# Optimization experiments

Hardware: AMD Instinct MI355X
Metric: run time of the kernel (lower is better)

Reference implementation:

```python
import jax, jax.numpy as jnp
import numpy as np

VOCAB = 1000
H = 500  # embedding_size == hidden_size
NEG_SLOPE = 0.01  # nn.LeakyReLU default


def lstm_last_hidden(tokens, emb, Wih, Whh, bih, bhh):
    # tokens: [N, L] int; returns final hidden state [N, H] (batch_first LSTM, h_T)
    x = emb[tokens]  # [N, L, H]
    N = x.shape[0]
    h0 = jnp.zeros((N, H), x.dtype)

    def step(carry, xt):
        h, c = carry
        gates = xt @ Wih.T + h @ Whh.T + bih + bhh  # [N, 4H], torch gate order i,f,g,o
        i, f, g, o = jnp.split(gates, 4, axis=-1)
        c = jax.nn.sigmoid(f) * c + jax.nn.sigmoid(i) * jnp.tanh(g)
        h = jax.nn.sigmoid(o) * jnp.tanh(c)
        return (h, c), None

    (h, _), _ = jax.lax.scan(step, (h0, h0), jnp.swapaxes(x, 0, 1))
    return h


def setup_inputs() -> dict:
    key = jax.random.key(0)
    ks = jax.random.split(key, 16)
    B, L, NH = 256, 128, 2048
    goals = jax.random.randint(ks[0], (B, L), 0, VOCAB, dtype=jnp.int32)
    hyps = jax.random.randint(ks[1], (NH, L), 0, VOCAB, dtype=jnp.int32)
    segment_ids = jnp.sort(jax.random.randint(ks[2], (NH,), 0, B, dtype=jnp.int32))
    s = 1.0 / np.sqrt(H)
    emb = jax.random.normal(ks[3], (VOCAB, H), jnp.float32)
    Wih = jax.random.uniform(ks[4], (4 * H, H), jnp.float32, -s, s)
    Whh = jax.random.uniform(ks[5], (4 * H, H), jnp.float32, -s, s)
    bih = jax.random.uniform(ks[6], (4 * H,), jnp.float32, -s, s)
    bhh = jax.random.uniform(ks[7], (4 * H,), jnp.float32, -s, s)
    s1 = 1.0 / np.sqrt(2 * H)
    W1 = jax.random.uniform(ks[8], (H, 2 * H), jnp.float32, -s1, s1)
    b1 = jax.random.uniform(ks[9], (H,), jnp.float32, -s1, s1)
    W2 = jax.random.uniform(ks[10], (H, H), jnp.float32, -s, s)
    b2 = jax.random.uniform(ks[11], (H,), jnp.float32, -s, s)
    Wf = jax.random.uniform(ks[12], (H, H), jnp.float32, -s, s)
    bf = jax.random.uniform(ks[13], (H,), jnp.float32, -s, s)
    return {"goals": goals, "hyps": hyps, "segment_ids": segment_ids,
            "emb": emb, "Wih": Wih, "Whh": Whh, "bih": bih, "bhh": bhh,
            "W1": W1, "b1": b1, "W2": W2, "b2": b2, "Wf": Wf, "bf": bf}


def reference(goals, hyps, segment_ids, emb, Wih, Whh, bih, bhh, W1, b1, W2, b2, Wf, bf):
    B = goals.shape[0]
    g = lstm_last_hidden(goals, emb, Wih, Whh, bih, bhh)      # [B, H]
    h = lstm_last_hidden(hyps, emb, Wih, Whh, bih, bhh)       # [NH, H]
    hyp_sum = jax.ops.segment_sum(h, segment_ids, num_segments=B)  # [B, H]
    x = jnp.concatenate([g, hyp_sum], axis=1)                  # [B, 2H]
    lrelu = lambda z: jnp.where(z >= 0, z, NEG_SLOPE * z)
    x = lrelu(x @ W1.T + b1)
    x = lrelu(x @ W2.T + b2)
    x = x @ Wf.T + bf
    norm = jnp.maximum(jnp.linalg.norm(x, axis=1, keepdims=True), 1e-12)
    return x / norm
```

## Files before the change

kernel.cpp:

```cpp
#include <hip/hip_runtime.h>
#include <hip/hip_bf16.h>

#define HH 500
#define G4 2000
#define NSEQ 2304
#define NGOALS 256
#define NHYPS 2048
#define LSEQ 128
#define NVOCAB 1000
#define NEG_SLOPE 0.01f

typedef __attribute__((ext_vector_type(4))) float f32x4;
typedef __attribute__((ext_vector_type(8))) short short8;

__device__ __forceinline__ float sigm(float x) { return 1.0f / (1.0f + expf(-x)); }

__device__ __forceinline__ void gload_lds16(const void* g, void* l) {
    __builtin_amdgcn_global_load_lds(
        (const __attribute__((address_space(1))) unsigned int*)g,
        (__attribute__((address_space(3))) unsigned int*)l, 16, 0, 0);
}

__global__ void gemm_at_bt(const float* __restrict__ A, const float* __restrict__ B,
                           const float* __restrict__ bias, const float* __restrict__ bias2,
                           float* __restrict__ C, int M, int N, int K, int act)
{
    __shared__ float as[32][17];
    __shared__ float bs[32][17];
    int tid = threadIdx.x;
    int tx = tid & 15, ty = tid >> 4;
    int m0 = blockIdx.y * 32, n0 = blockIdx.x * 32;
    float acc[2][2] = {};
    for (int k0 = 0; k0 < K; k0 += 16) {
        #pragma unroll
        for (int i = 0; i < 2; ++i) {
            int idx = i * 256 + tid;
            int r = idx >> 4, k = idx & 15;
            int gm = m0 + r, gk = k0 + k;
            as[r][k] = (gm < M && gk < K) ? A[gm * K + gk] : 0.0f;
            int gn = n0 + r;
            bs[r][k] = (gn < N && gk < K) ? B[gn * K + gk] : 0.0f;
        }
        __syncthreads();
        #pragma unroll
        for (int kk = 0; kk < 16; ++kk) {
            float a0 = as[ty][kk], a1 = as[ty + 16][kk];
            float b0 = bs[tx][kk], b1 = bs[tx + 16][kk];
            acc[0][0] += a0 * b0; acc[0][1] += a0 * b1;
            acc[1][0] += a1 * b0; acc[1][1] += a1 * b1;
        }
        __syncthreads();
    }
    #pragma unroll
    for (int i = 0; i < 2; ++i) {
        int m = m0 + ty + i * 16;
        if (m >= M) continue;
        #pragma unroll
        for (int j = 0; j < 2; ++j) {
            int n = n0 + tx + j * 16;
            if (n >= N) continue;
            float v = acc[i][j];
            if (bias)  v += bias[n];
            if (bias2) v += bias2[n];
            if (act == 1) v = (v >= 0.0f) ? v : NEG_SLOPE * v;
            C[m * N + n] = v;
        }
    }
}

__global__ void conv_whh(const float* __restrict__ Whh, __hip_bfloat16* __restrict__ Wb)
{
    int idx = blockIdx.x * 256 + threadIdx.x;
    if (idx >= 4 * 512 * 512) return;
    int k = idx & 511, u = (idx >> 9) & 511, g = idx >> 18;
    float v = (u < HH && k < HH) ? Whh[(g * HH + u) * HH + k] : 0.0f;
    Wb[idx] = __float2bfloat16(v);
}

__global__ __launch_bounds__(256) void lstm_step_mfma(
    const float* __restrict__ T,
    const int* __restrict__ goals, const int* __restrict__ hyps,
    const __hip_bfloat16* __restrict__ Wb,
    const __hip_bfloat16* __restrict__ hin,
    __hip_bfloat16* __restrict__ hout,
    float* __restrict__ c, int t)
{
    __shared__ char lds[20480];
    char* As = lds;
    char* Bs = lds + 4096;
    int tid = threadIdx.x, w = tid >> 6, lane = tid & 63;
    int n0 = blockIdx.y * 32, u0 = blockIdx.x * 32;
    f32x4 acc[4] = {};

    int lrow = lane >> 3;
    int cblk = (lane & 7) ^ lrow;
    const short* hin_s = (const short*)hin;
    const short* wb_s  = (const short*)Wb;

    int nsub = (w >> 1) * 16, usub = (w & 1) * 16;
    int arow = nsub + (lane & 15);
    int r7 = lane & 7;

    for (int k0 = 0; k0 < 512; k0 += 64) {
        gload_lds16(hin_s + (size_t)(n0 + w * 8 + lrow) * 512 + k0 + cblk * 8,
                    As + w * 1024);
        #pragma unroll
        for (int i = 0; i < 4; ++i) {
            int r = (i * 4 + w) * 8 + lrow;
            int g = r >> 5, u = u0 + (r & 31);
            gload_lds16(wb_s + (size_t)(g * 512 + u) * 512 + k0 + cblk * 8,
                        Bs + (i * 4 + w) * 1024);
        }
        __syncthreads();
        #pragma unroll
        for (int ks = 0; ks < 2; ++ks) {
            int blk = (ks * 4 + (lane >> 4)) ^ r7;
            short8 a = *(const short8*)(As + arow * 128 + blk * 16);
            #pragma unroll
            for (int g = 0; g < 4; ++g) {
                int br = g * 32 + usub + (lane & 15);
                short8 b = *(const short8*)(Bs + br * 128 + blk * 16);
                acc[g] = __builtin_amdgcn_mfma_f32_16x16x32_bf16(a, b, acc[g], 0, 0, 0);
            }
        }
        __syncthreads();
    }

    int u = u0 + usub + (lane & 15);
    if (u < HH) {
        #pragma unroll
        for (int r = 0; r < 4; ++r) {
            int n = n0 + nsub + (lane >> 4) * 4 + r;
            int tok = (n < NGOALS) ? goals[n * LSEQ + t] : hyps[(n - NGOALS) * LSEQ + t];
            const float* Trow = T + (size_t)tok * G4;
            float gi = acc[0][r] + Trow[u];
            float gf = acc[1][r] + Trow[HH + u];
            float gg = acc[2][r] + Trow[2 * HH + u];
            float go = acc[3][r] + Trow[3 * HH + u];
            float si = sigm(gi), sf = sigm(gf), so = sigm(go);
            float cv = c[(size_t)n * 512 + u];
            cv = sf * cv + si * tanhf(gg);
            c[(size_t)n * 512 + u] = cv;
            hout[(size_t)n * 512 + u] = __float2bfloat16(so * tanhf(cv));
        }
    }
}

__global__ void segsum_bf(const __hip_bfloat16* __restrict__ hfin,
                          const int* __restrict__ segid, float* __restrict__ hyp_sum)
{
    int row = blockIdx.y;
    int u = blockIdx.x * 256 + threadIdx.x;
    if (u >= HH) return;
    int b = segid[row];
    atomicAdd(&hyp_sum[b * HH + u],
              __bfloat162float(hfin[(size_t)(NGOALS + row) * 512 + u]));
}

__global__ void concat_bf(const __hip_bfloat16* __restrict__ hfin,
                          const float* __restrict__ hyp_sum, float* __restrict__ xcat)
{
    int r = blockIdx.y;
    int k = blockIdx.x * 256 + threadIdx.x;
    if (k >= 2 * HH) return;
    xcat[r * 2 * HH + k] = (k < HH) ? __bfloat162float(hfin[(size_t)r * 512 + k])
                                    : hyp_sum[r * HH + (k - HH)];
}

__global__ void rownorm(const float* __restrict__ X, float* __restrict__ out)
{
    __shared__ float red[256];
    int r = blockIdx.x;
    int tid = threadIdx.x;
    float v0 = (tid < HH) ? X[r * HH + tid] : 0.0f;
    float v1 = (tid + 256 < HH) ? X[r * HH + tid + 256] : 0.0f;
    red[tid] = v0 * v0 + v1 * v1;
    __syncthreads();
    for (int st = 128; st > 0; st >>= 1) {
        if (tid < st) red[tid] += red[tid + st];
        __syncthreads();
    }
    float nrm = fmaxf(sqrtf(red[0]), 1e-12f);
    if (tid < HH) out[r * HH + tid] = v0 / nrm;
    if (tid + 256 < HH) out[r * HH + tid + 256] = v1 / nrm;
}

extern "C" void kernel_launch(void* const* d_in, const int* in_sizes, int n_in,
                              void* d_out, int out_size, void* d_ws, size_t ws_size,
                              hipStream_t stream)
{
    const int*   goals = (const int*)d_in[0];
    const int*   hyps  = (const int*)d_in[1];
    const int*   segid = (const int*)d_in[2];
    const float* emb   = (const float*)d_in[3];
    const float* Wih   = (const float*)d_in[4];
    const float* Whh   = (const float*)d_in[5];
    const float* bih   = (const float*)d_in[6];
    const float* bhh   = (const float*)d_in[7];
    const float* W1    = (const float*)d_in[8];
    const float* b1    = (const float*)d_in[9];
    const float* W2    = (const float*)d_in[10];
    const float* b2    = (const float*)d_in[11];
    const float* Wf    = (const float*)d_in[12];
    const float* bf    = (const float*)d_in[13];
    float* out = (float*)d_out;

    char* base = (char*)d_ws;
    float*          T    = (float*)(base + 0);
    __hip_bfloat16* Wb   = (__hip_bfloat16*)(base + 8000000);
    __hip_bfloat16* hb0  = (__hip_bfloat16*)(base + 10097152);
    __hip_bfloat16* hb1  = (__hip_bfloat16*)(base + 12456448);
    float*          c    = (float*)(base + 14815744);
    float*          hsum = (float*)(base + 19534336);
    float*          xcat = (float*)(base + 20046336);
    float*          x1   = (float*)(base + 21070336);
    float*          x2   = (float*)(base + 21582336);

    gemm_at_bt<<<dim3((G4 + 31) / 32, (NVOCAB + 31) / 32), 256, 0, stream>>>(
        emb, Wih, bih, bhh, T, NVOCAB, G4, HH, 0);
    conv_whh<<<4096, 256, 0, stream>>>(Whh, Wb);

    hipMemsetAsync(hb0,  0, 2359296, stream);
    hipMemsetAsync(hb1,  0, 2359296, stream);
    hipMemsetAsync(c,    0, 4718592, stream);
    hipMemsetAsync(hsum, 0,  512000, stream);

    __hip_bfloat16* hb[2] = { hb0, hb1 };
    for (int t = 0; t < LSEQ; ++t) {
        lstm_step_mfma<<<dim3(16, NSEQ / 32), 256, 0, stream>>>(
            T, goals, hyps, Wb, hb[t & 1], hb[(t + 1) & 1], c, t);
    }
    __hip_bfloat16* hfin = hb0;

    segsum_bf<<<dim3(2, NHYPS), 256, 0, stream>>>(hfin, segid, hsum);
    concat_bf<<<dim3(4, NGOALS), 256, 0, stream>>>(hfin, hsum, xcat);

    gemm_at_bt<<<dim3(16, 8), 256, 0, stream>>>(xcat, W1, b1, nullptr, x1, NGOALS, HH, 2 * HH, 1);
    gemm_at_bt<<<dim3(16, 8), 256, 0, stream>>>(x1,   W2, b2, nullptr, x2, NGOALS, HH, HH, 1);
    gemm_at_bt<<<dim3(16, 8), 256, 0, stream>>>(x2,   Wf, bf, nullptr, xcat, NGOALS, HH, HH, 0);
    rownorm<<<NGOALS, 256, 0, stream>>>(xcat, out);
}
```

Baseline: 2.333 ms.

## Retile LSTM step with 32x32 MFMA double-buffered single-wave blocks and split-bf16 table GEMM

Replaces the per-step recurrent kernel with a single-wavefront block that computes a 64x(4x32) tile using 32x32x16 bf16 MFMAs. Global-to-LDS loads are double-buffered so the next K chunk loads while the current one is computed. The input-projection table is now built with a bf16 hi/lo split MFMA GEMM instead of the scalar fp32 GEMM, and its rows are padded to 512 columns per gate. The step kernel now launches 576 single-wave blocks each step, which lowers occupancy per CU and raises register pressure from the larger accumulators.

```diff
diff --git a/kernel.cpp b/kernel.cpp
--- a/kernel.cpp
+++ b/kernel.cpp
@@ -10,8 +10,9 @@
 #define NVOCAB 1000
 #define NEG_SLOPE 0.01f
 
-typedef __attribute__((ext_vector_type(4))) float f32x4;
-typedef __attribute__((ext_vector_type(8))) short short8;
+typedef __attribute__((ext_vector_type(4)))  float f32x4;
+typedef __attribute__((ext_vector_type(16))) float f32x16;
+typedef __attribute__((ext_vector_type(8)))  short short8;
 
 __device__ __forceinline__ float sigm(float x) { return 1.0f / (1.0f + expf(-x)); }
 
@@ -19,6 +20,182 @@
     __builtin_amdgcn_global_load_lds(
         (const __attribute__((address_space(1))) unsigned int*)g,
         (__attribute__((address_space(3))) unsigned int*)l, 16, 0, 0);
+}
+
+__global__ void split_emb(const float* __restrict__ emb,
+                          __hip_bfloat16* __restrict__ Eh, __hip_bfloat16* __restrict__ El)
+{
+    int idx = blockIdx.x * 256 + threadIdx.x;
+    if (idx >= 1024 * 512) return;
+    int k = idx & 511, r = idx >> 9;
+    float v = (r < NVOCAB && k < HH) ? emb[r * HH + k] : 0.0f;
+    __hip_bfloat16 h = __float2bfloat16(v);
+    Eh[idx] = h;
+    El[idx] = __float2bfloat16(v - __bfloat162float(h));
+}
+
+__global__ void split_wih(const float* __restrict__ Wih,
+                          __hip_bfloat16* __restrict__ Wh, __hip_bfloat16* __restrict__ Wl)
+{
+    int idx = blockIdx.x * 256 + threadIdx.x;
+    if (idx >= 2000 * 512) return;
+    int k = idx & 511, r = idx >> 9;
+    float v = (k < HH) ? Wih[r * HH + k] : 0.0f;
+    __hip_bfloat16 h = __float2bfloat16(v);
+    Wh[idx] = h;
+    Wl[idx] = __float2bfloat16(v - __bfloat162float(h));
+}
+
+__global__ void conv_whh(const float* __restrict__ Whh, __hip_bfloat16* __restrict__ Wb)
+{
+    int idx = blockIdx.x * 256 + threadIdx.x;
+    if (idx >= 4 * 512 * 512) return;
+    int k = idx & 511, u = (idx >> 9) & 511, g = idx >> 18;
+    float v = (u < HH && k < HH) ? Whh[(g * HH + u) * HH + k] : 0.0f;
+    Wb[idx] = __float2bfloat16(v);
+}
+
+__global__ __launch_bounds__(256) void tgemm_split(
+    const __hip_bfloat16* __restrict__ Eh, const __hip_bfloat16* __restrict__ El,
+    const __hip_bfloat16* __restrict__ Wh, const __hip_bfloat16* __restrict__ Wl,
+    const float* __restrict__ bih, const float* __restrict__ bhh,
+    float* __restrict__ T4)
+{
+    __shared__ char lds[40960];
+    int tid = threadIdx.x, w = tid >> 6, lane = tid & 63;
+    int j0 = blockIdx.x * 16;
+    int m0 = blockIdx.y * 64;
+    int lrow = lane >> 3, cblk = (lane & 7) ^ lrow, r7 = lane & 7;
+    const short* eh = (const short*)Eh; const short* el = (const short*)El;
+    const short* wh = (const short*)Wh; const short* wl = (const short*)Wl;
+    f32x4 acc = {};
+    int arow = w * 16 + (lane & 15);
+
+    auto STAGE = [&](int buf, int k0) {
+        char* base = lds + buf * 20480;
+        #pragma unroll
+        for (int i = 0; i < 2; ++i) {
+            int r = (w * 2 + i) * 8 + lrow;
+            gload_lds16(eh + (size_t)(m0 + r) * 512 + k0 + cblk * 8, base + (w * 2 + i) * 1024);
+            gload_lds16(el + (size_t)(m0 + r) * 512 + k0 + cblk * 8, base + 8192 + (w * 2 + i) * 1024);
+        }
+        {
+            int half = w & 1;
+            int r = half * 8 + lrow;
+            const short* src = (w < 2) ? wh : wl;
+            int off = (w < 2) ? 16384 : 18432;
+            gload_lds16(src + (size_t)(j0 + r) * 512 + 0 + cblk * 8 + k0, base + off + half * 1024);
+        }
+    };
+
+    STAGE(0, 0);
+    __syncthreads();
+    int cur = 0;
+    for (int ch = 0; ch < 8; ++ch) {
+        if (ch < 7) STAGE(cur ^ 1, (ch + 1) * 64);
+        char* base = lds + cur * 20480;
+        #pragma unroll
+        for (int ks = 0; ks < 2; ++ks) {
+            int blk = (ks * 4 + (lane >> 4)) ^ r7;
+            short8 ah = *(const short8*)(base + arow * 128 + blk * 16);
+            short8 al = *(const short8*)(base + 8192 + arow * 128 + blk * 16);
+            short8 bh = *(const short8*)(base + 16384 + (lane & 15) * 128 + blk * 16);
+            short8 bl = *(const short8*)(base + 18432 + (lane & 15) * 128 + blk * 16);
+            acc = __builtin_amdgcn_mfma_f32_16x16x32_bf16(ah, bh, acc, 0, 0, 0);
+            acc = __builtin_amdgcn_mfma_f32_16x16x32_bf16(ah, bl, acc, 0, 0, 0);
+            acc = __builtin_amdgcn_mfma_f32_16x16x32_bf16(al, bh, acc, 0, 0, 0);
+        }
+        if (ch < 7) { __syncthreads(); cur ^= 1; }
+    }
+    int j = j0 + (lane & 15);
+    int g = (j >= 1500) ? 3 : (j >= 1000) ? 2 : (j >= 500) ? 1 : 0;
+    int u = j - g * 500;
+    float bias = bih[j] + bhh[j];
+    #pragma unroll
+    for (int r = 0; r < 4; ++r) {
+        int m = m0 + w * 16 + (lane >> 4) * 4 + r;
+        if (m < NVOCAB) T4[(size_t)m * 2048 + g * 512 + u] = acc[r] + bias;
+    }
+}
+
+__global__ __launch_bounds__(64) void lstm_step3(
+    const float* __restrict__ T4,
+    const int* __restrict__ goals, const int* __restrict__ hyps,
+    const __hip_bfloat16* __restrict__ Wb,
+    const __hip_bfloat16* __restrict__ hin,
+    __hip_bfloat16* __restrict__ hout,
+    float* __restrict__ c, int tstep)
+{
+    __shared__ char lds[49152];
+    int lane = threadIdx.x;
+    int u0 = blockIdx.x * 32, n0 = blockIdx.y * 64;
+    int lrow = lane >> 3, l7 = lane & 7;
+    const short* hin_s = (const short*)hin;
+    const short* wb_s  = (const short*)Wb;
+    f32x16 acc[2][4] = {};
+
+    auto STAGE = [&](int buf, int k0) {
+        char* As_ = lds + buf * 24576;
+        char* Bs_ = As_ + 8192;
+        #pragma unroll
+        for (int i = 0; i < 8; ++i) {
+            int cb = l7 ^ lrow ^ (i & 3);
+            gload_lds16(hin_s + (size_t)(n0 + i * 8 + lrow) * 512 + k0 + cb * 8, As_ + i * 1024);
+        }
+        #pragma unroll
+        for (int i = 0; i < 16; ++i) {
+            int cb = l7 ^ lrow ^ (i & 3);
+            int r = i * 8 + lrow;
+            int g = r >> 5, uu = r & 31;
+            gload_lds16(wb_s + (size_t)(g * 512 + u0 + uu) * 512 + k0 + cb * 8, Bs_ + i * 1024);
+        }
+    };
+
+    STAGE(0, 0);
+    __syncthreads();
+    int cur = 0;
+    int l31 = lane & 31;
+    int keybase = l7 ^ ((lane >> 3) & 3);
+    for (int ch = 0; ch < 8; ++ch) {
+        if (ch < 7) STAGE(cur ^ 1, (ch + 1) * 64);
+        char* As_ = lds + cur * 24576;
+        char* Bs_ = As_ + 8192;
+        #pragma unroll
+        for (int ks = 0; ks < 4; ++ks) {
+            int blk = (ks * 2 + (lane >> 5)) ^ keybase;
+            short8 a0 = *(const short8*)(As_ + l31 * 128 + blk * 16);
+            short8 a1 = *(const short8*)(As_ + (32 + l31) * 128 + blk * 16);
+            #pragma unroll
+            for (int g = 0; g < 4; ++g) {
+                short8 b = *(const short8*)(Bs_ + (g * 32 + l31) * 128 + blk * 16);
+                acc[0][g] = __builtin_amdgcn_mfma_f32_32x32x16_bf16(a0, b, acc[0][g], 0, 0, 0);
+                acc[1][g] = __builtin_amdgcn_mfma_f32_32x32x16_bf16(a1, b, acc[1][g], 0, 0, 0);
+            }
+        }
+        if (ch < 7) { __syncthreads(); cur ^= 1; }
+    }
+
+    int u = u0 + l31;
+    if (u < HH) {
+        #pragma unroll
+        for (int r = 0; r < 2; ++r) {
+            #pragma unroll
+            for (int reg = 0; reg < 16; ++reg) {
+                int n = n0 + r * 32 + (reg & 3) + 8 * (reg >> 2) + 4 * (lane >> 5);
+                int tok = (n < NGOALS) ? goals[n * LSEQ + tstep] : hyps[(n - NGOALS) * LSEQ + tstep];
+                const float* Tg = T4 + (size_t)tok * 2048;
+                float gi = acc[r][0][reg] + Tg[u];
+                float gf = acc[r][1][reg] + Tg[512 + u];
+                float gg = acc[r][2][reg] + Tg[1024 + u];
+                float go = acc[r][3][reg] + Tg[1536 + u];
+                float si = sigm(gi), sf = sigm(gf), so = sigm(go);
+                float cv = c[(size_t)n * 512 + u];
+                cv = sf * cv + si * tanhf(gg);
+                c[(size_t)n * 512 + u] = cv;
+                hout[(size_t)n * 512 + u] = __float2bfloat16(so * tanhf(cv));
+            }
+        }
+    }
 }
 
 __global__ void gemm_at_bt(const float* __restrict__ A, const float* __restrict__ B,
@@ -64,84 +241,6 @@
             if (bias2) v += bias2[n];
             if (act == 1) v = (v >= 0.0f) ? v : NEG_SLOPE * v;
             C[m * N + n] = v;
-        }
-    }
-}
-
-__global__ void conv_whh(const float* __restrict__ Whh, __hip_bfloat16* __restrict__ Wb)
-{
-    int idx = blockIdx.x * 256 + threadIdx.x;
-    if (idx >= 4 * 512 * 512) return;
-    int k = idx & 511, u = (idx >> 9) & 511, g = idx >> 18;
-    float v = (u < HH && k < HH) ? Whh[(g * HH + u) * HH + k] : 0.0f;
-    Wb[idx] = __float2bfloat16(v);
-}
-
-__global__ __launch_bounds__(256) void lstm_step_mfma(
-    const float* __restrict__ T,
-    const int* __restrict__ goals, const int* __restrict__ hyps,
-    const __hip_bfloat16* __restrict__ Wb,
-    const __hip_bfloat16* __restrict__ hin,
-    __hip_bfloat16* __restrict__ hout,
-    float* __restrict__ c, int t)
-{
-    __shared__ char lds[20480];
-    char* As = lds;
-    char* Bs = lds + 4096;
-    int tid = threadIdx.x, w = tid >> 6, lane = tid & 63;
-    int n0 = blockIdx.y * 32, u0 = blockIdx.x * 32;
-    f32x4 acc[4] = {};
-
-    int lrow = lane >> 3;
-    int cblk = (lane & 7) ^ lrow;
-    const short* hin_s = (const short*)hin;
-    const short* wb_s  = (const short*)Wb;
-
-    int nsub = (w >> 1) * 16, usub = (w & 1) * 16;
-    int arow = nsub + (lane & 15);
-    int r7 = lane & 7;
-
-    for (int k0 = 0; k0 < 512; k0 += 64) {
-        gload_lds16(hin_s + (size_t)(n0 + w * 8 + lrow) * 512 + k0 + cblk * 8,
-                    As + w * 1024);
-        #pragma unroll
-        for (int i = 0; i < 4; ++i) {
-            int r = (i * 4 + w) * 8 + lrow;
-            int g = r >> 5, u = u0 + (r & 31);
-            gload_lds16(wb_s + (size_t)(g * 512 + u) * 512 + k0 + cblk * 8,
-                        Bs + (i * 4 + w) * 1024);
-        }
-        __syncthreads();
-        #pragma unroll
-        for (int ks = 0; ks < 2; ++ks) {
-            int blk = (ks * 4 + (lane >> 4)) ^ r7;
-            short8 a = *(const short8*)(As + arow * 128 + blk * 16);
-            #pragma unroll
-            for (int g = 0; g < 4; ++g) {
-                int br = g * 32 + usub + (lane & 15);
-                short8 b = *(const short8*)(Bs + br * 128 + blk * 16);
-                acc[g] = __builtin_amdgcn_mfma_f32_16x16x32_bf16(a, b, acc[g], 0, 0, 0);
-            }
-        }
-        __syncthreads();
-    }
-
-    int u = u0 + usub + (lane & 15);
-    if (u < HH) {
-        #pragma unroll
-        for (int r = 0; r < 4; ++r) {
-            int n = n0 + nsub + (lane >> 4) * 4 + r;
-            int tok = (n < NGOALS) ? goals[n * LSEQ + t] : hyps[(n - NGOALS) * LSEQ + t];
-            const float* Trow = T + (size_t)tok * G4;
-            float gi = acc[0][r] + Trow[u];
-            float gf = acc[1][r] + Trow[HH + u];
-            float gg = acc[2][r] + Trow[2 * HH + u];
-            float go = acc[3][r] + Trow[3 * HH + u];
-            float si = sigm(gi), sf = sigm(gf), so = sigm(go);
-            float cv = c[(size_t)n * 512 + u];
-            cv = sf * cv + si * tanhf(gg);
-            c[(size_t)n * 512 + u] = cv;
-            hout[(size_t)n * 512 + u] = __float2bfloat16(so * tanhf(cv));
         }
     }
 }
@@ -206,19 +305,24 @@
     float* out = (float*)d_out;
 
     char* base = (char*)d_ws;
-    float*          T    = (float*)(base + 0);
-    __hip_bfloat16* Wb   = (__hip_bfloat16*)(base + 8000000);
-    __hip_bfloat16* hb0  = (__hip_bfloat16*)(base + 10097152);
-    __hip_bfloat16* hb1  = (__hip_bfloat16*)(base + 12456448);
-    float*          c    = (float*)(base + 14815744);
-    float*          hsum = (float*)(base + 19534336);
-    float*          xcat = (float*)(base + 20046336);
-    float*          x1   = (float*)(base + 21070336);
-    float*          x2   = (float*)(base + 21582336);
-
-    gemm_at_bt<<<dim3((G4 + 31) / 32, (NVOCAB + 31) / 32), 256, 0, stream>>>(
-        emb, Wih, bih, bhh, T, NVOCAB, G4, HH, 0);
+    float*          T4   = (float*)(base + 0);
+    __hip_bfloat16* Wb   = (__hip_bfloat16*)(base + 8192000);
+    __hip_bfloat16* hb0  = (__hip_bfloat16*)(base + 10289152);
+    __hip_bfloat16* hb1  = (__hip_bfloat16*)(base + 12648448);
+    float*          c    = (float*)(base + 15007744);
+    float*          hsum = (float*)(base + 19726336);
+    float*          xcat = (float*)(base + 20238336);
+    float*          x1   = (float*)(base + 21262336);
+    float*          x2   = (float*)(base + 21774336);
+    __hip_bfloat16* Eh = (__hip_bfloat16*)(base + 10289152);
+    __hip_bfloat16* El = (__hip_bfloat16*)(base + 11337728);
+    __hip_bfloat16* Wh = (__hip_bfloat16*)(base + 12648448);
+    __hip_bfloat16* Wl = (__hip_bfloat16*)(base + 15007744);
+
+    split_emb<<<2048, 256, 0, stream>>>(emb, Eh, El);
+    split_wih<<<4000, 256, 0, stream>>>(Wih, Wh, Wl);
     conv_whh<<<4096, 256, 0, stream>>>(Whh, Wb);
+    tgemm_split<<<dim3(125, 16), 256, 0, stream>>>(Eh, El, Wh, Wl, bih, bhh, T4);
 
     hipMemsetAsync(hb0,  0, 2359296, stream);
     hipMemsetAsync(hb1,  0, 2359296, stream);
@@ -227,8 +331,8 @@
 
     __hip_bfloat16* hb[2] = { hb0, hb1 };
     for (int t = 0; t < LSEQ; ++t) {
-        lstm_step_mfma<<<dim3(16, NSEQ / 32), 256, 0, stream>>>(
-            T, goals, hyps, Wb, hb[t & 1], hb[(t + 1) & 1], c, t);
+        lstm_step3<<<dim3(16, 36), 64, 0, stream>>>(
+            T4, goals, hyps, Wb, hb[t & 1], hb[(t + 1) & 1], c, t);
     }
     __hip_bfloat16* hfin = hb0;
 
```

New measurement: 4.939 ms. +111.7%, slower.
